# Kernel tuning notes

Hardware: AMD Instinct MI355X
Metric: run time of the kernel (lower is better)

## Reference

```python
import jax, jax.numpy as jnp
import numpy as np

NUM_HEADS = 8
SPLIT_S = 4
DIM = 288            # n_feat * 3 * 3
SCALE = (DIM // NUM_HEADS) ** -0.5  # quirk: uses full dim's head_dim (36), not reduced
EPS = 1e-5


def _extract_patches(x):
    # x: [B,C,H,W] -> [B, C*9, H*W], 3x3 kernel, stride 1, 'same' padding
    B, C, H, W = x.shape
    xp = jnp.pad(x, ((0, 0), (0, 0), (1, 1), (1, 1)))
    pats = jnp.stack([xp[:, :, i:i + H, j:j + W] for i in range(3) for j in range(3)], axis=2)
    return pats.reshape(B, C * 9, H * W)


def _fold(cols, H, W):
    # inverse of extract: [B, C*9, H*W] -> [B,C,H,W], summing overlapping patches
    B, Ck, _ = cols.shape
    C = Ck // 9
    p = cols.reshape(B, C, 3, 3, H, W)
    out = jnp.zeros((B, C, H + 2, W + 2), cols.dtype)
    for i in range(3):
        for j in range(3):
            out = out.at[:, :, i:i + H, j:j + W].add(p[:, :, i, j])
    return out[:, :, 1:H + 1, 1:W + 1]


def _ln(x, w, b):
    mu = x.mean(-1, keepdims=True)
    var = ((x - mu) ** 2).mean(-1, keepdims=True)
    return (x - mu) * jax.lax.rsqrt(var + EPS) * w + b


def _attn(x, reduce_w, qkv_w, proj_w, proj_b):
    # x: [B,N,288] -> reduce -> [B,N,144] -> block-diag attention over s=4 chunks
    x = x @ reduce_w.T
    B, N, C = x.shape
    hd = C // NUM_HEADS
    qkv = (x @ qkv_w.T).reshape(B, N, 3, NUM_HEADS, hd).transpose(2, 0, 3, 1, 4)
    q, k, v = qkv[0], qkv[1], qkv[2]          # [B,h,N,hd]
    chunk = N // SPLIT_S
    q = q.reshape(B, NUM_HEADS, SPLIT_S, chunk, hd)
    k = k.reshape(B, NUM_HEADS, SPLIT_S, chunk, hd)
    v = v.reshape(B, NUM_HEADS, SPLIT_S, chunk, hd)
    attn = jnp.einsum('bhscd,bhsed->bhsce', q, k) * SCALE   # [B,h,s,chunk,chunk]
    attn = jax.nn.softmax(attn, axis=-1)
    out = jnp.einsum('bhsce,bhsed->bhscd', attn, v)          # [B,h,s,chunk,hd]
    out = out.transpose(0, 2, 3, 1, 4).reshape(B, N, C)      # cat chunks on token dim
    return out @ proj_w.T + proj_b


def setup_inputs() -> dict:
    key = jax.random.key(0)
    ks = jax.random.split(key, 12)
    d, dr, dh = DIM, DIM // 2, DIM // 4  # 288, 144, 72
    f = lambda k, shape: (jax.random.normal(k, shape, jnp.float32) * 0.02)
    return {
        'x': jax.random.normal(ks[0], (4, 32, 64, 64), jnp.float32),
        'ln1_w': jnp.ones((d,), jnp.float32), 'ln1_b': jnp.zeros((d,), jnp.float32),
        'reduce_w': f(ks[1], (dr, d)),
        'qkv_w': f(ks[2], (3 * dr, dr)),
        'proj_w': f(ks[3], (d, dr)), 'proj_b': jnp.zeros((d,), jnp.float32),
        'ln2_w': jnp.ones((d,), jnp.float32), 'ln2_b': jnp.zeros((d,), jnp.float32),
        'fc1_w': f(ks[4], (dh, d)), 'fc1_b': jnp.zeros((dh,), jnp.float32),
        'fc2_w': f(ks[5], (d, dh)), 'fc2_b': jnp.zeros((d,), jnp.float32),
    }


def reference(x, ln1_w, ln1_b, reduce_w, qkv_w, proj_w, proj_b, ln2_w, ln2_b, fc1_w, fc1_b, fc2_w, fc2_b):
    B, C, H, W = x.shape
    t = _extract_patches(x).transpose(0, 2, 1)  # [B, N=H*W, 288]
    t = t + _attn(_ln(t, ln1_w, ln1_b), reduce_w, qkv_w, proj_w, proj_b)
    h = _ln(t, ln2_w, ln2_b)
    t = t + (jax.nn.relu(h @ fc1_w.T + fc1_b) @ fc2_w.T + fc2_b)
    return _fold(t.transpose(0, 2, 1), H, W)
```

## Files before the change

### kernel.cpp

```cpp
#include <hip/hip_runtime.h>
#include <hip/hip_bf16.h>

typedef __hip_bfloat16 bf16;
typedef unsigned short u16;
typedef unsigned int u32;
typedef __attribute__((ext_vector_type(8))) short bf16x8;
typedef __attribute__((ext_vector_type(4))) float f32x4;

#define BB 4
#define CCH 32
#define HH 64
#define WW 64
#define NN 4096
#define D 288
#define DR 144
#define DQ 432
#define NH 8
#define HD 18
#define SPLIT 4
#define CHUNK 1024
#define NKSL 4
#define KS 256
#define DH 72
#define SCALE_ 0.16666666666666666f
#define QSCALE 0.24044917348149343f
#define EPS_ 1e-5f
#define ASTR 160
#define ATS 168
#define HSTR 96

__device__ __attribute__((aligned(16))) u16 g_Wcb[DQ * D];
__device__ __attribute__((aligned(16))) u16 g_pw[D * ASTR];
__device__ __attribute__((aligned(16))) u16 g_f1w[HSTR * D];
__device__ __attribute__((aligned(16))) u16 g_f2w[D * HSTR];
__device__ __attribute__((aligned(16))) u16 g_q[(size_t)BB * NH * NN * 32];
__device__ __attribute__((aligned(16))) u16 g_k[(size_t)BB * NH * NN * 32];
__device__ __attribute__((aligned(16))) u16 g_vt[(size_t)BB * NH * SPLIT * 32 * CHUNK];
__device__ __attribute__((aligned(16))) float g_part[NKSL * (size_t)BB * NH * NN * 20];
__device__ __attribute__((aligned(16))) u16 g_t0[(size_t)BB * NN * D];
__device__ __attribute__((aligned(16))) u16 g_t2b[(size_t)BB * D * NN];
__device__ int   g_flag;

__device__ __forceinline__ float b2f(bf16 v) { return __bfloat162float(v); }
__device__ __forceinline__ float bits2f(u16 u) { return __uint_as_float(((u32)u) << 16); }
__device__ __forceinline__ u16 f2bits(float f) {
    u32 u = __float_as_uint(f);
    return (u16)((u + 0x7FFF + ((u >> 16) & 1)) >> 16);
}
__device__ __forceinline__ float ldin(const void* p, size_t i, int isbf) {
    return isbf ? b2f(((const bf16*)p)[i]) : ((const float*)p)[i];
}
__device__ __forceinline__ u32 packexp(float e0, float e1) {
    float p0 = __builtin_amdgcn_exp2f(e0);
    float p1 = __builtin_amdgcn_exp2f(e1);
    return __builtin_amdgcn_perm(__float_as_uint(p1), __float_as_uint(p0), 0x07060302u);
}

#define RS  (D * ASTR + HSTR * D + D * HSTR)
#define RS2 (RS + BB * NH * SPLIT * CHUNK)
#define RSB ((RS2 + 255) / 256)
#define PATCHB (BB * HH)

__global__ void k_prep(const void* __restrict__ x, const void* __restrict__ qkv_w,
                       const void* __restrict__ reduce_w, const void* __restrict__ proj_w,
                       const void* __restrict__ fc1_w, const void* __restrict__ fc2_w) {
    __shared__ int cnt4[4];
    __shared__ float qw[DR];
    __shared__ float slab[32 * 3 * 66];
    int tid = threadIdx.x;
    {
        const u16* u = (const u16*)x;
        int c = 0;
        for (int i = tid; i < 2048; i += 256) c += (((u[i] >> 7) & 0xFF) >= 0x90);
        for (int o = 32; o; o >>= 1) c += __shfl_xor(c, o);
        if ((tid & 63) == 0) cnt4[tid >> 6] = c;
    }
    __syncthreads();
    int bf = (cnt4[0] + cnt4[1] + cnt4[2] + cnt4[3]) < 32;
    if (tid == 0 && blockIdx.x == 0) g_flag = bf;

    int bid = blockIdx.x;
    if (bid < DQ) {
        int o = bid;
        if (tid < DR) qw[tid] = ldin(qkv_w, (size_t)o * DR + tid, bf);
        __syncthreads();
        for (int col = tid; col < D; col += 256) {
            float s0 = 0.f, s1 = 0.f;
            #pragma unroll 4
            for (int j = 0; j < DR; j += 2) {
                s0 += qw[j] * ldin(reduce_w, (size_t)j * D + col, bf);
                s1 += qw[j + 1] * ldin(reduce_w, (size_t)(j + 1) * D + col, bf);
            }
            g_Wcb[(size_t)o * D + col] = f2bits(s0 + s1);
        }
    } else if (bid < DQ + RSB) {
        int idx = (bid - DQ) * 256 + tid;
        if (idx < D * ASTR) {
            int o = idx / ASTR, j = idx % ASTR;
            g_pw[idx] = (j < DR) ? f2bits(ldin(proj_w, (size_t)o * DR + j, bf)) : (u16)0;
        } else if (idx < D * ASTR + HSTR * D) {
            int t = idx - D * ASTR;
            int o = t / D;
            g_f1w[t] = (o < DH) ? f2bits(ldin(fc1_w, (size_t)t, bf)) : (u16)0;
        } else if (idx < RS) {
            int t = idx - D * ASTR - HSTR * D;
            int o = t / HSTR, j = t % HSTR;
            g_f2w[t] = (j < DH) ? f2bits(ldin(fc2_w, (size_t)o * DH + j, bf)) : (u16)0;
        } else if (idx < RS2) {
            int t = idx - RS;
            int bhs = t >> 10, n = t & 1023;
            g_vt[((size_t)bhs * 32 + 18) * CHUNK + n] = 0x3F80;
        }
    } else {
        int pb = bid - DQ - RSB;
        int b = pb >> 6, y = pb & 63;
        for (int idx = tid; idx < 32 * 3 * 66; idx += 256) {
            int c = idx / 198, rem = idx % 198;
            int ki = rem / 66, col = rem % 66 - 1;
            int sy = y + ki - 1;
            float v = 0.f;
            if (col >= 0 && col < 64 && sy >= 0 && sy < 64)
                v = ldin(x, ((size_t)(b * CCH + c) * HH + sy) * WW + col, bf);
            slab[idx] = v;
        }
        __syncthreads();
        size_t obase = ((size_t)b * NN + y * 64) * D;
        for (int idx = tid; idx < 64 * D; idx += 256) {
            int t = idx / D, f = idx % D;
            int c = f / 9, k = f % 9, ki = k / 3, kj = k % 3;
            g_t0[obase + idx] = f2bits(slab[c * 198 + ki * 66 + t + kj]);
        }
    }
}

__global__ void k_ln_qkv(const void* __restrict__ lnw, const void* __restrict__ lnb) {
    __shared__ __attribute__((aligned(16))) u16 xln[32 * 296];
    __shared__ float lnwf[D], lnbf[D];
    __shared__ float smu[32], srs[32];
    __shared__ u16 buf[3][144][32];
    int bf = g_flag;
    int tid = threadIdx.x;
    size_t tok0 = (size_t)blockIdx.x * 32;
    for (int i = tid; i < D; i += 256) { lnwf[i] = ldin(lnw, i, bf); lnbf[i] = ldin(lnb, i, bf); }
    {
        int tt = tid >> 3, p = tid & 7;
        const u32* pr = (const u32*)(g_t0 + (tok0 + tt) * D + p * 36);
        float s = 0.f, q = 0.f;
        #pragma unroll
        for (int j = 0; j < 18; ++j) {
            u32 v = pr[j];
            float a = bits2f((u16)(v & 0xFFFF)), b = bits2f((u16)(v >> 16));
            s += a + b; q += a * a + b * b;
        }
        #pragma unroll
        for (int o = 1; o < 8; o <<= 1) { s += __shfl_xor(s, o); q += __shfl_xor(q, o); }
        if (p == 0) {
            float mu = s / D;
            smu[tt] = mu;
            srs[tt] = rsqrtf(q / D - mu * mu + EPS_);
        }
    }
    __syncthreads();
    for (int idx = tid; idx < 32 * 144; idx += 256) {
        int t = idx / 144, dw = idx % 144;
        u32 v = *(const u32*)(g_t0 + (tok0 + t) * D + 2 * dw);
        float mu = smu[t], rs = srs[t];
        int f = 2 * dw;
        float a = (bits2f((u16)(v & 0xFFFF)) - mu) * rs * lnwf[f] + lnbf[f];
        float b = (bits2f((u16)(v >> 16)) - mu) * rs * lnwf[f + 1] + lnbf[f + 1];
        *(u32*)&xln[t * 296 + f] = (u32)f2bits(a) | ((u32)f2bits(b) << 16);
    }
    __syncthreads();
    int w = tid >> 6, lane = tid & 63, quad = lane >> 4, l15 = lane & 15;
    bf16x8 areg0[9], areg1[9];
    {
        const u16* a0 = xln + l15 * 296 + quad * 8;
        const u16* a1 = xln + (16 + l15) * 296 + quad * 8;
        #pragma unroll
        for (int ks = 0; ks < 9; ++ks) {
            areg0[ks] = *(const bf16x8*)(a0 + ks * 32);
            areg1[ks] = *(const bf16x8*)(a1 + ks * 32);
        }
    }
    int nt0 = w * 7, nt1 = (nt0 + 7 > 27) ? 27 : nt0 + 7;
    for (int nt = nt0; nt < nt1; ++nt) {
        f32x4 acc0 = {0.f, 0.f, 0.f, 0.f}, acc1 = {0.f, 0.f, 0.f, 0.f};
        const u16* bbase = g_Wcb + (size_t)(nt * 16 + l15) * D + quad * 8;
        #pragma unroll
        for (int ks = 0; ks < 9; ++ks) {
            bf16x8 bfr = *(const bf16x8*)(bbase + ks * 32);
            acc0 = __builtin_amdgcn_mfma_f32_16x16x32_bf16(areg0[ks], bfr, acc0, 0, 0, 0);
            acc1 = __builtin_amdgcn_mfma_f32_16x16x32_bf16(areg1[ks], bfr, acc1, 0, 0, 0);
        }
        int o = nt * 16 + l15;
        int which = o / DR, rem = o % DR;
        #pragma unroll
        for (int r = 0; r < 4; ++r) {
            buf[which][rem][quad * 4 + r] = f2bits(which == 0 ? acc0[r] * QSCALE : acc0[r]);
            buf[which][rem][16 + quad * 4 + r] = f2bits(which == 0 ? acc1[r] * QSCALE : acc1[r]);
        }
    }
    __syncthreads();
    {
        int b_ = (int)(tok0 >> 12);
        int n0 = (int)(tok0 & 4095);
        int sIdx = n0 >> 10, nc = n0 & 1023;
        for (int idx = tid; idx < 2 * 8 * 32 * 9; idx += 256) {
            int which = idx / 2304;
            int r2 = idx - which * 2304;
            int h = r2 / 288, r3 = r2 % 288, t = r3 / 9, dw = r3 % 9;
            u32 lo = buf[which][h * 18 + 2 * dw][t];
            u32 hi = buf[which][h * 18 + 2 * dw + 1][t];
            u16* dst = (which ? g_k : g_q) + ((size_t)(b_ * NH + h) * NN + n0 + t) * 32 + 2 * dw;
            *(u32*)dst = lo | (hi << 16);
        }
        for (int idx = tid; idx < 144 * 16; idx += 256) {
            int rem = idx >> 4, tp = idx & 15;
            int hh = rem / HD, dd = rem % HD;
            u32 lo = buf[2][rem][2 * tp];
            u32 hi = buf[2][rem][2 * tp + 1];
            int k2 = 2 * tp;
            int pos = 8 * ((k2 >> 2) & 3) + 4 * (k2 >> 4) + (k2 & 3);
            size_t voff = (((size_t)(b_ * NH + hh) * SPLIT + sIdx) * 32 + dd) * CHUNK + nc + pos;
            *(u32*)&g_vt[voff] = lo | (hi << 16);
        }
    }
}

__global__ __launch_bounds__(128, 4) void k_attn() {
    int bid = blockIdx.x;
    int chunk = bid & 127;
    int qblk = (bid >> 7) & 7;
    int ksl = bid >> 10;
    int s = chunk & 3, bh = chunk >> 2;
    int tid = threadIdx.x;
    int w = tid >> 6, lane = tid & 63, quad = lane >> 4, l15 = lane & 15;

    size_t rowbase = (size_t)bh * NN + s * CHUNK;
    size_t vtbase = ((size_t)bh * SPLIT + s) * 32 * CHUNK;
    const u16* kbase = g_k + rowbase * 32 + quad * 8;
    const u16* vbase = g_vt + vtbase + quad * 8;

    int qbase = qblk * 128 + w * 64;
    bf16x8 qf[4];
    #pragma unroll
    for (int t = 0; t < 4; ++t)
        qf[t] = *(const bf16x8*)(g_q + (rowbase + qbase + t * 16 + l15) * 32 + quad * 8);

    f32x4 accA[4], accB[4];
    #pragma unroll
    for (int t = 0; t < 4; ++t) {
        accA[t] = (f32x4){0.f, 0.f, 0.f, 0.f};
        accB[t] = (f32x4){0.f, 0.f, 0.f, 0.f};
    }

    int kt0 = ksl * KS;

    auto loadK = [&](bf16x8 (&dst)[4], int kt) {
        dst[0] = *(const bf16x8*)(kbase + (size_t)(kt + l15) * 32);
        dst[1] = *(const bf16x8*)(kbase + (size_t)(kt + 16 + l15) * 32);
        dst[2] = *(const bf16x8*)(kbase + (size_t)(kt + 32 + l15) * 32);
        dst[3] = *(const bf16x8*)(kbase + (size_t)(kt + 48 + l15) * 32);
    };
    auto body = [&](bf16x8 (&kc)[4], bf16x8 (&kn)[4], int kt, bool pf) {
        bf16x8 vA0 = *(const bf16x8*)(vbase + (size_t)l15 * CHUNK + kt);
        bf16x8 vB0 = *(const bf16x8*)(vbase + (size_t)(16 + l15) * CHUNK + kt);
        bf16x8 vA1 = *(const bf16x8*)(vbase + (size_t)l15 * CHUNK + kt + 32);
        bf16x8 vB1 = *(const bf16x8*)(vbase + (size_t)(16 + l15) * CHUNK + kt + 32);
        if (pf) loadK(kn, kt + 64);
        f32x4 z = {0.f, 0.f, 0.f, 0.f};
        #pragma unroll
        for (int t = 0; t < 4; ++t) {
            __builtin_amdgcn_s_setprio(1);
            f32x4 S0 = __builtin_amdgcn_mfma_f32_16x16x32_bf16(kc[0], qf[t], z, 0, 0, 0);
            f32x4 S1 = __builtin_amdgcn_mfma_f32_16x16x32_bf16(kc[1], qf[t], z, 0, 0, 0);
            f32x4 S2 = __builtin_amdgcn_mfma_f32_16x16x32_bf16(kc[2], qf[t], z, 0, 0, 0);
            f32x4 S3 = __builtin_amdgcn_mfma_f32_16x16x32_bf16(kc[3], qf[t], z, 0, 0, 0);
            __builtin_amdgcn_s_setprio(0);
            union { u32 u[4]; bf16x8 v; } pa0, pa1;
            pa0.u[0] = packexp(S0[0], S0[1]);
            pa0.u[1] = packexp(S0[2], S0[3]);
            pa0.u[2] = packexp(S1[0], S1[1]);
            pa0.u[3] = packexp(S1[2], S1[3]);
            pa1.u[0] = packexp(S2[0], S2[1]);
            pa1.u[1] = packexp(S2[2], S2[3]);
            pa1.u[2] = packexp(S3[0], S3[1]);
            pa1.u[3] = packexp(S3[2], S3[3]);
            __builtin_amdgcn_s_setprio(1);
            accA[t] = __builtin_amdgcn_mfma_f32_16x16x32_bf16(pa0.v, vA0, accA[t], 0, 0, 0);
            accB[t] = __builtin_amdgcn_mfma_f32_16x16x32_bf16(pa0.v, vB0, accB[t], 0, 0, 0);
            accA[t] = __builtin_amdgcn_mfma_f32_16x16x32_bf16(pa1.v, vA1, accA[t], 0, 0, 0);
            accB[t] = __builtin_amdgcn_mfma_f32_16x16x32_bf16(pa1.v, vB1, accB[t], 0, 0, 0);
            __builtin_amdgcn_s_setprio(0);
        }
    };

    bf16x8 ka[4], kb[4];
    loadK(ka, kt0);
    body(ka, kb, kt0, true);
    body(kb, ka, kt0 + 64, true);
    body(ka, kb, kt0 + 128, true);
    body(kb, ka, kt0 + 192, false);

    float* pb = g_part + (((size_t)ksl * 32 + bh) * SPLIT + s) * (size_t)(CHUNK * 20);
    #pragma unroll
    for (int t = 0; t < 4; ++t) {
        #pragma unroll
        for (int r = 0; r < 4; ++r) {
            int tokenc = qbase + t * 16 + quad * 4 + r;
            float* row = pb + (size_t)tokenc * 20;
            row[l15] = accA[t][r];
            if (l15 < 3) row[16 + l15] = accB[t][r];
        }
    }
}

__global__ void k_proj_mlp(const void* __restrict__ proj_b, const void* __restrict__ lnw,
                           const void* __restrict__ lnb, const void* __restrict__ fc1_b,
                           const void* __restrict__ fc2_b) {
    __shared__ __attribute__((aligned(16))) u16 t1f[32 * 296];
    __shared__ __attribute__((aligned(16))) u16 xln[32 * 296];
    __shared__ __attribute__((aligned(16))) u16 attnT[32 * ATS];
    __shared__ __attribute__((aligned(16))) u16 hbuf[32 * HSTR];
    __shared__ float lnwf[D], lnbf[D];
    __shared__ float smu[32], srs[32];
    int bf = g_flag;
    int tid = threadIdx.x;
    size_t tok0 = (size_t)blockIdx.x * 32;
    int w = tid >> 6, lane = tid & 63, quad = lane >> 4, l15 = lane & 15;
    for (int i = tid; i < D; i += 256) { lnwf[i] = ldin(lnw, i, bf); lnbf[i] = ldin(lnb, i, bf); }

    int b_ = (int)(tok0 >> 12);
    int s_ = ((int)tok0 & 4095) >> 10;
    int tc0 = (int)tok0 & 1023;
    for (int idx = tid; idx < 32 * (ATS - DR); idx += 256) {
        int t = idx / (ATS - DR), f = idx % (ATS - DR);
        attnT[t * ATS + DR + f] = 0;
    }
    {
        int t = tid >> 3, h = tid & 7;
        const float* p1 = g_part + (((size_t)(b_ * NH + h)) * SPLIT + s_) * (size_t)(CHUNK * 20)
                        + (size_t)(tc0 + t) * 20;
        const size_t SL = (size_t)32 * SPLIT * CHUNK * 20;
        f32x4 a0 = {0,0,0,0}, a1 = {0,0,0,0}, a2 = {0,0,0,0}, a3 = {0,0,0,0}, a4 = {0,0,0,0};
        #pragma unroll
        for (int sl = 0; sl < NKSL; ++sl) {
            const float* p = p1 + sl * SL;
            a0 += *(const f32x4*)p;
            a1 += *(const f32x4*)(p + 4);
            a2 += *(const f32x4*)(p + 8);
            a3 += *(const f32x4*)(p + 12);
            a4 += *(const f32x4*)(p + 16);
        }
        float inv = 1.f / a4[2];
        u16* dst = attnT + t * ATS + h * HD;
        #pragma unroll
        for (int d = 0; d < 4; ++d) {
            dst[d]      = f2bits(a0[d] * inv);
            dst[4 + d]  = f2bits(a1[d] * inv);
            dst[8 + d]  = f2bits(a2[d] * inv);
            dst[12 + d] = f2bits(a3[d] * inv);
        }
        dst[16] = f2bits(a4[0] * inv);
        dst[17] = f2bits(a4[1] * inv);
    }
    __syncthreads();

    {
        bf16x8 areg0[5], areg1[5];
        const u16* a0 = attnT + l15 * ATS + quad * 8;
        const u16* a1 = attnT + (16 + l15) * ATS + quad * 8;
        #pragma unroll
        for (int ks = 0; ks < 5; ++ks) {
            areg0[ks] = *(const bf16x8*)(a0 + ks * 32);
            areg1[ks] = *(const bf16x8*)(a1 + ks * 32);
        }
        const int tab[5] = {0, 5, 10, 14, 18};
        for (int nt = tab[w]; nt < tab[w + 1]; ++nt) {
            f32x4 acc0 = {0.f, 0.f, 0.f, 0.f}, acc1 = {0.f, 0.f, 0.f, 0.f};
            const u16* bbase = g_pw + (size_t)(nt * 16 + l15) * ASTR + quad * 8;
            #pragma unroll
            for (int ks = 0; ks < 5; ++ks) {
                bf16x8 bfr = *(const bf16x8*)(bbase + ks * 32);
                acc0 = __builtin_amdgcn_mfma_f32_16x16x32_bf16(areg0[ks], bfr, acc0, 0, 0, 0);
                acc1 = __builtin_amdgcn_mfma_f32_16x16x32_bf16(areg1[ks], bfr, acc1, 0, 0, 0);
            }
            int o = nt * 16 + l15;
            float bias = ldin(proj_b, o, bf);
            #pragma unroll
            for (int r = 0; r < 4; ++r) {
                t1f[(quad * 4 + r) * 296 + o] =
                    f2bits(bits2f(g_t0[(tok0 + quad * 4 + r) * D + o]) + acc0[r] + bias);
                t1f[(16 + quad * 4 + r) * 296 + o] =
                    f2bits(bits2f(g_t0[(tok0 + 16 + quad * 4 + r) * D + o]) + acc1[r] + bias);
            }
        }
    }
    __syncthreads();
    {
        int tt = tid >> 3, p = tid & 7;
        const u32* src = (const u32*)&t1f[tt * 296 + p * 36];
        float s = 0.f, q = 0.f;
        #pragma unroll
        for (int j = 0; j < 18; ++j) {
            u32 v = src[j];
            float a = bits2f((u16)(v & 0xFFFF)), b = bits2f((u16)(v >> 16));
            s += a + b; q += a * a + b * b;
        }
        #pragma unroll
        for (int o = 1; o < 8; o <<= 1) { s += __shfl_xor(s, o); q += __shfl_xor(q, o); }
        if (p == 0) {
            float mu = s / D;
            smu[tt] = mu;
            srs[tt] = rsqrtf(q / D - mu * mu + EPS_);
        }
    }
    __syncthreads();
    for (int idx = tid; idx < 32 * 144; idx += 256) {
        int t = idx / 144, dw = idx % 144;
        int f = 2 * dw;
        u32 v = *(const u32*)&t1f[t * 296 + f];
        float mu = smu[t], rs = srs[t];
        float a = (bits2f((u16)(v & 0xFFFF)) - mu) * rs * lnwf[f] + lnbf[f];
        float b = (bits2f((u16)(v >> 16)) - mu) * rs * lnwf[f + 1] + lnbf[f + 1];
        *(u32*)&xln[t * 296 + f] = (u32)f2bits(a) | ((u32)f2bits(b) << 16);
    }
    __syncthreads();
    {
        bf16x8 areg0[9], areg1[9];
        const u16* a0 = xln + l15 * 296 + quad * 8;
        const u16* a1 = xln + (16 + l15) * 296 + quad * 8;
        #pragma unroll
        for (int ks = 0; ks < 9; ++ks) {
            areg0[ks] = *(const bf16x8*)(a0 + ks * 32);
            areg1[ks] = *(const bf16x8*)(a1 + ks * 32);
        }
        const int tab2[5] = {0, 2, 4, 5, 6};
        for (int nt = tab2[w]; nt < tab2[w + 1]; ++nt) {
            f32x4 acc0 = {0.f, 0.f, 0.f, 0.f}, acc1 = {0.f, 0.f, 0.f, 0.f};
            const u16* bbase = g_f1w + (size_t)(nt * 16 + l15) * D + quad * 8;
            #pragma unroll
            for (int ks = 0; ks < 9; ++ks) {
                bf16x8 bfr = *(const bf16x8*)(bbase + ks * 32);
                acc0 = __builtin_amdgcn_mfma_f32_16x16x32_bf16(areg0[ks], bfr, acc0, 0, 0, 0);
                acc1 = __builtin_amdgcn_mfma_f32_16x16x32_bf16(areg1[ks], bfr, acc1, 0, 0, 0);
            }
            int o = nt * 16 + l15;
            float bias = (o < DH) ? ldin(fc1_b, o, bf) : 0.f;
            #pragma unroll
            for (int r = 0; r < 4; ++r) {
                hbuf[(quad * 4 + r) * HSTR + o] = f2bits(fmaxf(acc0[r] + bias, 0.f));
                hbuf[(16 + quad * 4 + r) * HSTR + o] = f2bits(fmaxf(acc1[r] + bias, 0.f));
            }
        }
    }
    __syncthreads();
    {
        bf16x8 areg0[3], areg1[3];
        const u16* a0 = hbuf + l15 * HSTR + quad * 8;
        const u16* a1 = hbuf + (16 + l15) * HSTR + quad * 8;
        #pragma unroll
        for (int ks = 0; ks < 3; ++ks) {
            areg0[ks] = *(const bf16x8*)(a0 + ks * 32);
            areg1[ks] = *(const bf16x8*)(a1 + ks * 32);
        }
        const int tab[5] = {0, 5, 10, 14, 18};
        for (int nt = tab[w]; nt < tab[w + 1]; ++nt) {
            f32x4 acc0 = {0.f, 0.f, 0.f, 0.f}, acc1 = {0.f, 0.f, 0.f, 0.f};
            const u16* bbase = g_f2w + (size_t)(nt * 16 + l15) * HSTR + quad * 8;
            #pragma unroll
            for (int ks = 0; ks < 3; ++ks) {
                bf16x8 bfr = *(const bf16x8*)(bbase + ks * 32);
                acc0 = __builtin_amdgcn_mfma_f32_16x16x32_bf16(areg0[ks], bfr, acc0, 0, 0, 0);
                acc1 = __builtin_amdgcn_mfma_f32_16x16x32_bf16(areg1[ks], bfr, acc1, 0, 0, 0);
            }
            int o = nt * 16 + l15;
            float bias = ldin(fc2_b, o, bf);
            #pragma unroll
            for (int r = 0; r < 4; ++r) {
                xln[(quad * 4 + r) * 296 + o] =
                    f2bits(bits2f(t1f[(quad * 4 + r) * 296 + o]) + acc0[r] + bias);
                xln[(16 + quad * 4 + r) * 296 + o] =
                    f2bits(bits2f(t1f[(16 + quad * 4 + r) * 296 + o]) + acc1[r] + bias);
            }
        }
    }
    __syncthreads();
    {
        int n0 = (int)(tok0 & 4095);
        for (int idx = tid; idx < D * 16; idx += 256) {
            int o = idx >> 4, tp = idx & 15;
            u32 v = (u32)xln[(2 * tp) * 296 + o] | ((u32)xln[(2 * tp + 1) * 296 + o] << 16);
            *(u32*)&g_t2b[((size_t)b_ * D + o) * NN + n0 + 2 * tp] = v;
        }
    }
}

__global__ void k_fold(void* __restrict__ out) {
    int bf = g_flag;
    int idx = blockIdx.x * blockDim.x + threadIdx.x;
    if (idx >= BB * CCH * HH * WW) return;
    int xx = idx % WW;
    int y = (idx / WW) % HH;
    int c = (idx / (WW * HH)) % CCH;
    int b = idx / (WW * HH * CCH);
    const u16* base = g_t2b + ((size_t)b * D + c * 9) * NN;
    float s = 0.f;
    #pragma unroll
    for (int i = 0; i < 3; ++i) {
        int sy = y + 1 - i;
        if (sy < 0 || sy >= HH) continue;
        #pragma unroll
        for (int j = 0; j < 3; ++j) {
            int sx = xx + 1 - j;
            if (sx < 0 || sx >= WW) continue;
            s += bits2f(base[(size_t)(i * 3 + j) * NN + sy * WW + sx]);
        }
    }
    if (bf) ((bf16*)out)[idx] = __float2bfloat16(s);
    else    ((float*)out)[idx] = s;
}

extern "C" void kernel_launch(void* const* d_in, const int* in_sizes, int n_in,
                              void* d_out, int out_size, void* d_ws, size_t ws_size,
                              hipStream_t stream) {
    const void* x        = d_in[0];
    const void* ln1_w    = d_in[1];
    const void* ln1_b    = d_in[2];
    const void* reduce_w = d_in[3];
    const void* qkv_w    = d_in[4];
    const void* proj_w   = d_in[5];
    const void* proj_b   = d_in[6];
    const void* ln2_w    = d_in[7];
    const void* ln2_b    = d_in[8];
    const void* fc1_w    = d_in[9];
    const void* fc1_b    = d_in[10];
    const void* fc2_w    = d_in[11];
    const void* fc2_b    = d_in[12];

    k_prep     <<<DQ + RSB + PATCHB, 256, 0, stream>>>(x, qkv_w, reduce_w, proj_w, fc1_w, fc2_w);
    k_ln_qkv   <<<BB * NN / 32, 256, 0, stream>>>(ln1_w, ln1_b);
    k_attn     <<<NKSL * BB * NH * SPLIT * 8, 128, 0, stream>>>();
    k_proj_mlp <<<BB * NN / 32, 256, 0, stream>>>(proj_b, ln2_w, ln2_b, fc1_b, fc2_b);
    k_fold     <<<(BB * CCH * HH * WW + 255) / 256, 256, 0, stream>>>(d_out);
}
```

Before: 195.3 us.

## Drop split-K in attention and normalize outputs in-kernel to bf16

Each attention block now loops over the full 1024-key chunk instead of one of four 256-key slices. It normalizes by the softmax denominator, taken from the accumulator lane via shuffle, and writes bf16 results directly. This removes the fp32 partial buffer, its write and readback, and the reduction in the proj/MLP kernel. The cost is a grid four times smaller, 1024 blocks of 128 threads, which means less parallelism and longer per-block latency.

```diff
diff --git a/kernel.cpp b/kernel.cpp
--- a/kernel.cpp
+++ b/kernel.cpp
@@ -19,8 +19,6 @@
 #define HD 18
 #define SPLIT 4
 #define CHUNK 1024
-#define NKSL 4
-#define KS 256
 #define DH 72
 #define SCALE_ 0.16666666666666666f
 #define QSCALE 0.24044917348149343f
@@ -36,7 +34,7 @@
 __device__ __attribute__((aligned(16))) u16 g_q[(size_t)BB * NH * NN * 32];
 __device__ __attribute__((aligned(16))) u16 g_k[(size_t)BB * NH * NN * 32];
 __device__ __attribute__((aligned(16))) u16 g_vt[(size_t)BB * NH * SPLIT * 32 * CHUNK];
-__device__ __attribute__((aligned(16))) float g_part[NKSL * (size_t)BB * NH * NN * 20];
+__device__ __attribute__((aligned(16))) u16 g_attn[(size_t)BB * NN * 144];
 __device__ __attribute__((aligned(16))) u16 g_t0[(size_t)BB * NN * D];
 __device__ __attribute__((aligned(16))) u16 g_t2b[(size_t)BB * D * NN];
 __device__ int   g_flag;
@@ -230,8 +228,7 @@
 __global__ __launch_bounds__(128, 4) void k_attn() {
     int bid = blockIdx.x;
     int chunk = bid & 127;
-    int qblk = (bid >> 7) & 7;
-    int ksl = bid >> 10;
+    int qblk = bid >> 7;
     int s = chunk & 3, bh = chunk >> 2;
     int tid = threadIdx.x;
     int w = tid >> 6, lane = tid & 63, quad = lane >> 4, l15 = lane & 15;
@@ -253,8 +250,6 @@
         accA[t] = (f32x4){0.f, 0.f, 0.f, 0.f};
         accB[t] = (f32x4){0.f, 0.f, 0.f, 0.f};
     }
-
-    int kt0 = ksl * KS;
 
     auto loadK = [&](bf16x8 (&dst)[4], int kt) {
         dst[0] = *(const bf16x8*)(kbase + (size_t)(kt + l15) * 32);
@@ -296,21 +291,25 @@
     };
 
     bf16x8 ka[4], kb[4];
-    loadK(ka, kt0);
-    body(ka, kb, kt0, true);
-    body(kb, ka, kt0 + 64, true);
-    body(ka, kb, kt0 + 128, true);
-    body(kb, ka, kt0 + 192, false);
-
-    float* pb = g_part + (((size_t)ksl * 32 + bh) * SPLIT + s) * (size_t)(CHUNK * 20);
+    loadK(ka, 0);
+    #pragma unroll
+    for (int it = 0; it < 8; ++it) {
+        body(ka, kb, it * 128, true);
+        body(kb, ka, it * 128 + 64, it < 7);
+    }
+
+    u16* abase = g_attn + ((size_t)(bh >> 3) * NN + s * CHUNK) * 144 + (bh & 7) * HD;
+    int srcl = (lane & 48) | 2;
     #pragma unroll
     for (int t = 0; t < 4; ++t) {
         #pragma unroll
         for (int r = 0; r < 4; ++r) {
-            int tokenc = qbase + t * 16 + quad * 4 + r;
-            float* row = pb + (size_t)tokenc * 20;
-            row[l15] = accA[t][r];
-            if (l15 < 3) row[16 + l15] = accB[t][r];
+            float den = __shfl(accB[t][r], srcl);
+            float inv = __builtin_amdgcn_rcpf(den);
+            int tc = qbase + t * 16 + quad * 4 + r;
+            u16* dst = abase + (size_t)tc * 144;
+            dst[l15] = f2bits(accA[t][r] * inv);
+            if (l15 < 2) dst[16 + l15] = f2bits(accB[t][r] * inv);
         }
     }
 }
@@ -331,38 +330,17 @@
     for (int i = tid; i < D; i += 256) { lnwf[i] = ldin(lnw, i, bf); lnbf[i] = ldin(lnb, i, bf); }
 
     int b_ = (int)(tok0 >> 12);
-    int s_ = ((int)tok0 & 4095) >> 10;
-    int tc0 = (int)tok0 & 1023;
+    int n0 = (int)(tok0 & 4095);
     for (int idx = tid; idx < 32 * (ATS - DR); idx += 256) {
         int t = idx / (ATS - DR), f = idx % (ATS - DR);
         attnT[t * ATS + DR + f] = 0;
     }
     {
-        int t = tid >> 3, h = tid & 7;
-        const float* p1 = g_part + (((size_t)(b_ * NH + h)) * SPLIT + s_) * (size_t)(CHUNK * 20)
-                        + (size_t)(tc0 + t) * 20;
-        const size_t SL = (size_t)32 * SPLIT * CHUNK * 20;
-        f32x4 a0 = {0,0,0,0}, a1 = {0,0,0,0}, a2 = {0,0,0,0}, a3 = {0,0,0,0}, a4 = {0,0,0,0};
-        #pragma unroll
-        for (int sl = 0; sl < NKSL; ++sl) {
-            const float* p = p1 + sl * SL;
-            a0 += *(const f32x4*)p;
-            a1 += *(const f32x4*)(p + 4);
-            a2 += *(const f32x4*)(p + 8);
-            a3 += *(const f32x4*)(p + 12);
-            a4 += *(const f32x4*)(p + 16);
-        }
-        float inv = 1.f / a4[2];
-        u16* dst = attnT + t * ATS + h * HD;
-        #pragma unroll
-        for (int d = 0; d < 4; ++d) {
-            dst[d]      = f2bits(a0[d] * inv);
-            dst[4 + d]  = f2bits(a1[d] * inv);
-            dst[8 + d]  = f2bits(a2[d] * inv);
-            dst[12 + d] = f2bits(a3[d] * inv);
-        }
-        dst[16] = f2bits(a4[0] * inv);
-        dst[17] = f2bits(a4[1] * inv);
+        const u16* src = g_attn + ((size_t)b_ * NN + n0) * 144;
+        for (int idx = tid; idx < 32 * 72; idx += 256) {
+            int t = idx / 72, dw = idx % 72;
+            *(u32*)&attnT[t * ATS + 2 * dw] = *(const u32*)&src[(size_t)t * 144 + 2 * dw];
+        }
     }
     __syncthreads();
 
@@ -487,7 +465,6 @@
     }
     __syncthreads();
     {
-        int n0 = (int)(tok0 & 4095);
         for (int idx = tid; idx < D * 16; idx += 256) {
             int o = idx >> 4, tp = idx & 15;
             u32 v = (u32)xln[(2 * tp) * 296 + o] | ((u32)xln[(2 * tp + 1) * 296 + o] << 16);
@@ -540,7 +517,7 @@
 
     k_prep     <<<DQ + RSB + PATCHB, 256, 0, stream>>>(x, qkv_w, reduce_w, proj_w, fc1_w, fc2_w);
     k_ln_qkv   <<<BB * NN / 32, 256, 0, stream>>>(ln1_w, ln1_b);
-    k_attn     <<<NKSL * BB * NH * SPLIT * 8, 128, 0, stream>>>();
+    k_attn     <<<BB * NH * SPLIT * 8, 128, 0, stream>>>();
     k_proj_mlp <<<BB * NN / 32, 256, 0, stream>>>(proj_b, ln2_w, ln2_b, fc1_b, fc2_b);
     k_fold     <<<(BB * CCH * HH * WW + 255) / 256, 256, 0, stream>>>(d_out);
 }
```

Result: faster. 182.2 us (-6.7%).
